# Performance work log

Measured on AMD Instinct MI355X. Metric: run time of the kernel, lower is better.

## Reference

```python
import jax, jax.numpy as jnp
import numpy as np

SQRT2 = 1.4142135623730951


def setup_inputs() -> dict:
    key = jax.random.key(0)
    kA, kW, kb = jax.random.split(key, 3)
    B = 2097152
    # Build SPD matrices: x = A A^T + 0.1 I  (well-conditioned, positive definite)
    A = jax.random.normal(kA, (B, 2, 2), dtype=jnp.float32)
    x = jnp.einsum('bik,bjk->bij', A, A) + 0.1 * jnp.eye(2, dtype=jnp.float32)
    # Linear(3, 17) params, torch default init scale 1/sqrt(fan_in)
    lim = 1.0 / np.sqrt(3.0)
    W = jax.random.uniform(kW, (17, 3), dtype=jnp.float32, minval=-lim, maxval=lim)
    b = jax.random.uniform(kb, (17,), dtype=jnp.float32, minval=-lim, maxval=lim)
    return {"x": x, "W": W, "b": b}


def reference(x, W, b):
    # SPD tangent space: matrix log via eigendecomposition of 2x2 SPD matrices
    w, V = jnp.linalg.eigh(x)                       # w: [B,2], V: [B,2,2]
    logw = jnp.log(w)
    L = jnp.einsum('bij,bj,bkj->bik', V, logw, V)    # log(x): [B,2,2] symmetric
    # Upper-triangular vectorization with sqrt(2) on off-diagonal -> [B,3]
    vec = jnp.stack([L[:, 0, 0], SQRT2 * L[:, 0, 1], L[:, 1, 1]], axis=-1)
    # Linear(3, 17)
    return vec @ W.T + b
```

## Files before the change

kernel.cpp:

```cpp
#include <hip/hip_runtime.h>


#define SQRT2F 1.41421356237309504880f

typedef float vfloat4 __attribute__((ext_vector_type(4)));

__global__ __launch_bounds__(512) void spd_log_linear_kernel(
    const vfloat4* __restrict__ x,
    const float*  __restrict__ W,
    const float*  __restrict__ bias,
    float*        __restrict__ out)
{
    __shared__ float sout[512 * 17];

    const int t = threadIdx.x;
    const long long gid = (long long)blockIdx.x * 512 + t;

    const vfloat4 xv = x[gid];
    const float a = xv.x, b = xv.y, c = xv.w;

    const float m    = 0.5f * (a + c);
    const float h    = 0.5f * (a - c);
    const float disc = sqrtf(fmaf(h, h, b * b));
    const float lam1 = m + disc;
    const float det  = fmaf(a, c, -b * b);
    const float lam2 = det / lam1;
    const float l1 = logf(lam1);
    const float l2 = logf(lam2);
    const float p  = 0.5f * (l1 + l2);
    const float q  = 0.5f * (l1 - l2);
    const float r  = (disc > 1e-20f) ? (q / disc) : (1.0f / m);

    const float v0 = p + r * h;
    const float v1 = SQRT2F * r * b;
    const float v2 = p - r * h;

    #pragma unroll
    for (int j = 0; j < 17; ++j) {
        sout[t * 17 + j] = fmaf(v0, W[j * 3 + 0],
                           fmaf(v1, W[j * 3 + 1],
                           fmaf(v2, W[j * 3 + 2], bias[j])));
    }
    __syncthreads();

    vfloat4* outv = (vfloat4*)(out + (long long)blockIdx.x * 8704);
    const vfloat4* sv = (const vfloat4*)sout;
    #pragma unroll
    for (int k = 0; k < 4; ++k) outv[t + k * 512] = sv[t + k * 512];
    if (t < 128) outv[2048 + t] = sv[2048 + t];
}

extern "C" void kernel_launch(void* const* d_in, const int* in_sizes, int n_in,
                              void* d_out, int out_size, void* d_ws, size_t ws_size,
                              hipStream_t stream) {
    const float* x = (const float*)d_in[0];
    const float* W = (const float*)d_in[1];
    const float* b = (const float*)d_in[2];
    float* out = (float*)d_out;

    const int B = in_sizes[0] / 4;
    const int blocks = B / 512;

    spd_log_linear_kernel<<<blocks, 512, 0, stream>>>(
        (const vfloat4*)x, W, b, out);
}
```

Measured before the change: 32.90 us.

## Compute each output float4 directly from its source matrices, dropping the shared-memory transpose

Each thread now produces one float4 of the output directly. It recomputes the matrix log for the one or two input rows that float4 spans, which replaces the per-thread 17-float shared staging buffer and its block-wide barrier. Weights and bias are packed into a small shared table read as float4, and the full-precision divides and logs are swapped for fast intrinsics. The cost is redundant log/eigen work and repeated input loads per row (about 4.25 evaluations per matrix), plus a hardcoded matrix count and a small loss of accuracy from the intrinsics.

Result: slower. 51.33 us (+56.0%).

```diff
diff --git a/kernel.cpp b/kernel.cpp
--- a/kernel.cpp
+++ b/kernel.cpp
@@ -2,52 +2,75 @@
 
 
 #define SQRT2F 1.41421356237309504880f
+#define NMAT   2097152
 
 typedef float vfloat4 __attribute__((ext_vector_type(4)));
 
-__global__ __launch_bounds__(512) void spd_log_linear_kernel(
-    const vfloat4* __restrict__ x,
-    const float*  __restrict__ W,
-    const float*  __restrict__ bias,
-    float*        __restrict__ out)
-{
-    __shared__ float sout[512 * 17];
-
-    const int t = threadIdx.x;
-    const long long gid = (long long)blockIdx.x * 512 + t;
-
-    const vfloat4 xv = x[gid];
+__device__ __forceinline__ void mat_log_vec(const vfloat4 xv,
+                                            float& v0, float& v1, float& v2) {
     const float a = xv.x, b = xv.y, c = xv.w;
-
     const float m    = 0.5f * (a + c);
     const float h    = 0.5f * (a - c);
     const float disc = sqrtf(fmaf(h, h, b * b));
     const float lam1 = m + disc;
     const float det  = fmaf(a, c, -b * b);
-    const float lam2 = det / lam1;
-    const float l1 = logf(lam1);
-    const float l2 = logf(lam2);
+    const float lam2 = __fdividef(det, lam1);
+    const float l1 = __logf(lam1);
+    const float l2 = __logf(lam2);
     const float p  = 0.5f * (l1 + l2);
     const float q  = 0.5f * (l1 - l2);
-    const float r  = (disc > 1e-20f) ? (q / disc) : (1.0f / m);
+    const float rho = (disc > 1e-20f) ? __fdividef(q, disc)
+                                      : __fdividef(1.0f, m);
+    v0 = fmaf(rho, h, p);
+    v1 = SQRT2F * rho * b;
+    v2 = fmaf(-rho, h, p);
+}
 
-    const float v0 = p + r * h;
-    const float v1 = SQRT2F * r * b;
-    const float v2 = p - r * h;
+__global__ __launch_bounds__(256) void spd_direct_kernel(
+    const vfloat4* __restrict__ x,
+    const float*   __restrict__ W,
+    const float*   __restrict__ bias,
+    vfloat4*       __restrict__ out)
+{
+    __shared__ float sWb[17][4];
 
-    #pragma unroll
-    for (int j = 0; j < 17; ++j) {
-        sout[t * 17 + j] = fmaf(v0, W[j * 3 + 0],
-                           fmaf(v1, W[j * 3 + 1],
-                           fmaf(v2, W[j * 3 + 2], bias[j])));
+    const int t = threadIdx.x;
+    if (t < 68) {
+        const int j = t >> 2, c = t & 3;
+        sWb[j][c] = (c < 3) ? W[j * 3 + c] : bias[j];
     }
     __syncthreads();
 
-    vfloat4* outv = (vfloat4*)(out + (long long)blockIdx.x * 8704);
-    const vfloat4* sv = (const vfloat4*)sout;
+    const int g0 = blockIdx.x * 1024 + t;
+
     #pragma unroll
-    for (int k = 0; k < 4; ++k) outv[t + k * 512] = sv[t + k * 512];
-    if (t < 128) outv[2048 + t] = sv[2048 + t];
+    for (int kk = 0; kk < 4; ++kk) {
+        const int g  = g0 + kk * 256;
+        const int f  = g * 4;
+        const int r0 = f / 17;
+        const int j0 = f - r0 * 17;
+        const int r1 = (r0 + 1 < NMAT) ? r0 + 1 : r0;
+
+        float a0, a1, a2, b0, b1, b2;
+        mat_log_vec(x[r0], a0, a1, a2);
+        mat_log_vec(x[r1], b0, b1, b2);
+
+        vfloat4 o;
+        #pragma unroll
+        for (int k = 0; k < 4; ++k) {
+            int j = j0 + k;
+            const bool hi = (j >= 17);
+            j -= hi ? 17 : 0;
+            const float u0 = hi ? b0 : a0;
+            const float u1 = hi ? b1 : a1;
+            const float u2 = hi ? b2 : a2;
+            const vfloat4 wb = *(const vfloat4*)&sWb[j][0];
+            const float r = fmaf(u0, wb.x, fmaf(u1, wb.y, fmaf(u2, wb.z, wb.w)));
+            if (k == 0) o.x = r; else if (k == 1) o.y = r;
+            else if (k == 2) o.z = r; else o.w = r;
+        }
+        out[g] = o;
+    }
 }
 
 extern "C" void kernel_launch(void* const* d_in, const int* in_sizes, int n_in,
@@ -58,9 +81,8 @@
     const float* b = (const float*)d_in[2];
     float* out = (float*)d_out;
 
-    const int B = in_sizes[0] / 4;
-    const int blocks = B / 512;
+    const int blocks = (out_size / 4) / 1024;
 
-    spd_log_linear_kernel<<<blocks, 512, 0, stream>>>(
-        (const vfloat4*)x, W, b, out);
+    spd_direct_kernel<<<blocks, 256, 0, stream>>>(
+        (const vfloat4*)x, W, b, (vfloat4*)d_out);
 }
```
